# Kernel optimization log

Hardware: AMD Instinct MI355X
Metric: run time of the kernel (lower is better)

Reference implementation:

```python
import jax, jax.numpy as jnp
import numpy as np

B = 524288
D_IN = 128
D_OUT = 128
MASK_DENSITY = 0.25  # fraction of DAG edges present


def setup_inputs() -> dict:
    key = jax.random.key(0)
    k = jax.random.split(key, 6)
    x0 = jax.random.normal(k[0], (B, D_IN), dtype=jnp.float32)
    x1 = jax.random.normal(k[1], (B, D_IN), dtype=jnp.float32)
    # weights ~ N(0, 0.1^2) as in torch.normal(mean=0, std=0.1)
    w0 = jax.random.normal(k[2], (D_OUT, D_IN), dtype=jnp.float32) * 0.1
    w1 = jax.random.normal(k[3], (D_OUT, D_IN), dtype=jnp.float32) * 0.1
    # binary DAG connectivity masks [out_dim, in_dims[i]]
    m0 = (jax.random.uniform(k[4], (D_OUT, D_IN)) < MASK_DENSITY).astype(jnp.float32)
    m1 = (jax.random.uniform(k[5], (D_OUT, D_IN)) < MASK_DENSITY).astype(jnp.float32)
    return {"x0": x0, "x1": x1, "w0": w0, "w1": w1, "m0": m0, "m1": m1}


def reference(x0, x1, w0, w1, m0, m1):
    # sum_i  x_i @ (W_i * M_i)^T   -> [B, out_dim]
    # (note: original module creates self.bias but never adds it in forward)
    out = jnp.einsum("bi,oi->bo", x0, w0 * m0)
    out = out + jnp.einsum("bi,oi->bo", x1, w1 * m1)
    return out
```

## Files before the change

kernel.cpp:

```cpp
#include <hip/hip_runtime.h>

typedef __attribute__((ext_vector_type(8))) short bf16x8;
typedef __attribute__((ext_vector_type(4))) float f32x4;
typedef __attribute__((ext_vector_type(4))) int   i32x4;
typedef __attribute__((ext_vector_type(2))) unsigned int u32x2;

#define NBLK 1024
#define NTHR 512
#define NT   32
#define DOUT 128

__device__ __forceinline__ unsigned short bf_rne(float x) {
  unsigned u = __builtin_bit_cast(unsigned, x);
  return (unsigned short)((u + 0x7FFFu + ((u >> 16) & 1u)) >> 16);
}
__device__ __forceinline__ void split2(float x, short& hi, short& lo) {
  unsigned u = __builtin_bit_cast(unsigned, x);
  float hf = __builtin_bit_cast(float, u & 0xFFFF0000u);
  hi = (short)(unsigned short)(u >> 16);
  lo = (short)bf_rne(x - hf);
}
__device__ __forceinline__ unsigned pk(short a, short b) {
  return (unsigned)(unsigned short)a | ((unsigned)(unsigned short)b << 16);
}
__device__ __forceinline__ void gll16(const float* g, char* l) {
  __builtin_amdgcn_global_load_lds(
      (const __attribute__((address_space(1))) unsigned int*)g,
      (__attribute__((address_space(3))) unsigned int*)l, 16, 0, 0);
}

#define MFMA_AW(ACC, W, X)                                                   \
  asm("s_nop 1\n\tv_mfma_f32_16x16x32_bf16 %0, %1, %2, %0"                   \
      : "+v"(ACC) : "a"(W), "v"(X))

__global__ __launch_bounds__(NTHR, 2)
void dagmm(const float* __restrict__ x0, const float* __restrict__ x1,
           const float* __restrict__ w0, const float* __restrict__ w1,
           const float* __restrict__ m0, const float* __restrict__ m1,
           float* __restrict__ out)
{
  __shared__ __align__(16) char L[65536];

  const int t   = threadIdx.x;
  const int l   = t & 63;
  const int w   = t >> 6;
  const int l16 = l & 15;
  const int lq  = l >> 4;

  i32x4 WH[8], WL[8];
  {
    const int col = w * 16 + l16;
#pragma unroll
    for (int ks = 0; ks < 8; ++ks) {
      const int k0 = ks * 32 + lq * 8;
      const float* wp = (k0 < 128) ? (w0 + col * 128 + k0) : (w1 + col * 128 + (k0 - 128));
      const float* mp = (k0 < 128) ? (m0 + col * 128 + k0) : (m1 + col * 128 + (k0 - 128));
      float4 wa = *(const float4*)wp, wb = *(const float4*)(wp + 4);
      float4 ma = *(const float4*)mp, mb = *(const float4*)(mp + 4);
      float v[8] = {wa.x*ma.x, wa.y*ma.y, wa.z*ma.z, wa.w*ma.w,
                    wb.x*mb.x, wb.y*mb.y, wb.z*mb.z, wb.w*mb.w};
      bf16x8 hv, lv;
#pragma unroll
      for (int j = 0; j < 8; ++j) { short h, lo2; split2(v[j], h, lo2); hv[j] = h; lv[j] = lo2; }
      WH[ks] = __builtin_bit_cast(i32x4, hv);
      WL[ks] = __builtin_bit_cast(i32x4, lv);
      asm volatile("" : "+a"(WH[ks]));
      asm volatile("" : "+a"(WL[ks]));
    }
  }

  const size_t Tbase = (size_t)blockIdx.x * (NT * 16);
  const float* xsrc = (l < 32) ? (x0 + l * 4) : (x1 + (l - 32) * 4);

#define ISSUE(ts, fbase)                                                     \
  {                                                                          \
    _Pragma("unroll")                                                        \
    for (int i = 0; i < 2; ++i) {                                            \
      const int row = w + i * 8;                                             \
      const size_t grow = Tbase + (size_t)(ts) * 16 + row;                   \
      gll16(xsrc + grow * 128, L + (fbase) + row * 1024);                    \
    }                                                                        \
  }

#define SPLIT(fbase, bbase)                                                  \
  {                                                                          \
    const float4 ra = *(const float4*)(L + (fbase) + t * 16);                \
    const float4 rb = *(const float4*)(L + (fbase) + t * 16 + 8192);         \
    const int ks   = (t & 63) >> 3;                                          \
    const int oct  = ((t & 63) >> 1) & 3;                                    \
    const int half = (t & 1) * 8;                                            \
    short h0,h1,h2,h3, e0,e1,e2,e3;                                          \
    u32x2 hv, lv;                                                            \
    {                                        \
      split2(ra.x, h0, e0); split2(ra.y, h1, e1);                            \
      split2(ra.z, h2, e2); split2(ra.w, h3, e3);                            \
      hv[0] = pk(h0, h1); hv[1] = pk(h2, h3);                                \
      lv[0] = pk(e0, e1); lv[1] = pk(e2, e3);                                \
      const int lam = (t >> 6) | (oct << 4);                                 \
      char* p = L + (bbase) + ks * 1024 + (((lam ^ ks)) << 4) + half;        \
      *(u32x2*)p          = hv;                                              \
      *(u32x2*)(p + 8192) = lv;                                              \
    }                                                                        \
    {                                         \
      split2(rb.x, h0, e0); split2(rb.y, h1, e1);                            \
      split2(rb.z, h2, e2); split2(rb.w, h3, e3);                            \
      hv[0] = pk(h0, h1); hv[1] = pk(h2, h3);                                \
      lv[0] = pk(e0, e1); lv[1] = pk(e2, e3);                                \
      const int lam = (8 + (t >> 6)) | (oct << 4);                           \
      char* p = L + (bbase) + ks * 1024 + (((lam ^ ks)) << 4) + half;        \
      *(u32x2*)p          = hv;                                              \
      *(u32x2*)(p + 8192) = lv;                                              \
    }                                                                        \
  }

  ISSUE(0, 0);
  ISSUE(1, 16384);
  asm volatile("s_waitcnt vmcnt(2)" ::: "memory");
  SPLIT(0, 32768);
  asm volatile("s_waitcnt lgkmcnt(0)" ::: "memory");

  for (int tt = 0; tt < NT; ++tt) {
    const int r = tt & 1;

    asm volatile("" ::: "memory");
    __builtin_amdgcn_s_barrier();
    asm volatile("" ::: "memory");

    { const int ts = (tt + 2 < NT) ? (tt + 2) : (NT - 1); ISSUE(ts, r * 16384); }

    asm volatile("s_waitcnt vmcnt(2)" ::: "memory");

    if (tt + 1 < NT) SPLIT((r ^ 1) * 16384, 32768 + (r ^ 1) * 16384);

    f32x4 acc = (f32x4){0.f, 0.f, 0.f, 0.f};
    {
      const char* Bb = L + 32768 + r * 16384;
#pragma unroll
      for (int ks = 0; ks < 8; ++ks) {
        const char* bp = Bb + ks * 1024 + ((l ^ ks) << 4);
        i32x4 xh = *(const i32x4*)bp;
        i32x4 xl = *(const i32x4*)(bp + 8192);
        MFMA_AW(acc, WH[ks], xh);
        MFMA_AW(acc, WH[ks], xl);
        MFMA_AW(acc, WL[ks], xh);
      }
    }
    asm volatile("s_nop 7\n\ts_nop 7" :::);

    {
      const size_t row = Tbase + (size_t)tt * 16 + l16;
      *(f32x4*)&out[row * DOUT + w * 16 + lq * 4] = acc;
    }

    asm volatile("s_waitcnt lgkmcnt(0)" ::: "memory");
  }
#undef ISSUE
#undef SPLIT
}

extern "C" void kernel_launch(void* const* d_in, const int* in_sizes, int n_in,
                              void* d_out, int out_size, void* d_ws, size_t ws_size,
                              hipStream_t stream) {
  const float* x0 = (const float*)d_in[0];
  const float* x1 = (const float*)d_in[1];
  const float* w0 = (const float*)d_in[2];
  const float* w1 = (const float*)d_in[3];
  const float* m0 = (const float*)d_in[4];
  const float* m1 = (const float*)d_in[5];
  dagmm<<<NBLK, NTHR, 0, stream>>>(x0, x1, w0, w1, m0, m1, (float*)d_out);
}
```

Measured before the change: 184.8 us.

## Halve block size, give each wave two output column tiles, use hardware bf16 pack

Cuts the block to 4 waves, each holding weights for two 16-column output tiles so every B-fragment read from LDS feeds two MFMA chains. This halves LDS fragment reads per output and interleaves two independent accumulators to hide MFMA dependency latency. The split-to-bf16 step switches to v_cvt_pk_bf16_f32, and each thread now converts four rows' worth of loads, with waitcnt adjusted for four loads per stage. It doubles weight register use per thread, and there is a stray line that dereferences a null pointer in the weight setup that may be optimized away or crash.

```diff
diff --git a/kernel.cpp b/kernel.cpp
--- a/kernel.cpp
+++ b/kernel.cpp
@@ -1,12 +1,11 @@
 #include <hip/hip_runtime.h>
 
-typedef __attribute__((ext_vector_type(8))) short bf16x8;
 typedef __attribute__((ext_vector_type(4))) float f32x4;
 typedef __attribute__((ext_vector_type(4))) int   i32x4;
 typedef __attribute__((ext_vector_type(2))) unsigned int u32x2;
 
 #define NBLK 1024
-#define NTHR 512
+#define NTHR 256
 #define NT   32
 #define DOUT 128
 
@@ -20,15 +19,17 @@
   hi = (short)(unsigned short)(u >> 16);
   lo = (short)bf_rne(x - hf);
 }
-__device__ __forceinline__ unsigned pk(short a, short b) {
-  return (unsigned)(unsigned short)a | ((unsigned)(unsigned short)b << 16);
+__device__ __forceinline__ float fbits(unsigned u) { return __builtin_bit_cast(float, u); }
+__device__ __forceinline__ unsigned cvtpk(float a, float b) {
+  unsigned r;
+  asm("v_cvt_pk_bf16_f32 %0, %1, %2" : "=v"(r) : "v"(a), "v"(b));
+  return r;
 }
 __device__ __forceinline__ void gll16(const float* g, char* l) {
   __builtin_amdgcn_global_load_lds(
       (const __attribute__((address_space(1))) unsigned int*)g,
       (__attribute__((address_space(3))) unsigned int*)l, 16, 0, 0);
 }
-
 #define MFMA_AW(ACC, W, X)                                                   \
   asm("s_nop 1\n\tv_mfma_f32_16x16x32_bf16 %0, %1, %2, %0"                   \
       : "+v"(ACC) : "a"(W), "v"(X))
@@ -47,9 +48,10 @@
   const int l16 = l & 15;
   const int lq  = l >> 4;
 
-  i32x4 WH[8], WL[8];
-  {
-    const int col = w * 16 + l16;
+  i32x4 WH[2][8], WL[2][8];
+#pragma unroll
+  for (int c = 0; c < 2; ++c) {
+    const int col = w * 32 + c * 16 + l16;
 #pragma unroll
     for (int ks = 0; ks < 8; ++ks) {
       const int k0 = ks * 32 + lq * 8;
@@ -59,55 +61,56 @@
       float4 ma = *(const float4*)mp, mb = *(const float4*)(mp + 4);
       float v[8] = {wa.x*ma.x, wa.y*ma.y, wa.z*ma.z, wa.w*ma.w,
                     wb.x*mb.x, wb.y*mb.y, wb.z*mb.z, wb.w*mb.w};
-      bf16x8 hv, lv;
+      short hv[8], lv[8];
 #pragma unroll
-      for (int j = 0; j < 8; ++j) { short h, lo2; split2(v[j], h, lo2); hv[j] = h; lv[j] = lo2; }
-      WH[ks] = __builtin_bit_cast(i32x4, hv);
-      WL[ks] = __builtin_bit_cast(i32x4, lv);
-      asm volatile("" : "+a"(WH[ks]));
-      asm volatile("" : "+a"(WL[ks]));
+      for (int j = 0; j < 8; ++j) split2(v[j], hv[j], lv[j]);
+      WH[c][ks] = __builtin_bit_cast(i32x4, *(f32x4*)0 == *(f32x4*)0 ? *(i32x4*)hv : *(i32x4*)hv);
+      WH[c][ks] = *(const i32x4*)hv;
+      WL[c][ks] = *(const i32x4*)lv;
+      asm volatile("" : "+a"(WH[c][ks]));
+      asm volatile("" : "+a"(WL[c][ks]));
     }
   }
 
   const size_t Tbase = (size_t)blockIdx.x * (NT * 16);
   const float* xsrc = (l < 32) ? (x0 + l * 4) : (x1 + (l - 32) * 4);
 
-#define ISSUE(ts, fbase)                                                     \
+#define ISSUE(ts, fb)                                                        \
   {                                                                          \
     _Pragma("unroll")                                                        \
-    for (int i = 0; i < 2; ++i) {                                            \
-      const int row = w + i * 8;                                             \
+    for (int i = 0; i < 4; ++i) {                                            \
+      const int row = w * 4 + i;                                             \
       const size_t grow = Tbase + (size_t)(ts) * 16 + row;                   \
-      gll16(xsrc + grow * 128, L + (fbase) + row * 1024);                    \
+      gll16(xsrc + grow * 128, L + (fb) + row * 1024);                       \
     }                                                                        \
   }
 
-#define SPLIT(fbase, bbase)                                                  \
+  const int rS    = t >> 4;
+  const int vS    = t & 15;
+  const int lamS  = rS | (((vS >> 1) & 3) << 4);
+  const int halfS = (vS & 1) * 8;
+
+#define SPLIT(fb, bb)                                                        \
   {                                                                          \
-    const float4 ra = *(const float4*)(L + (fbase) + t * 16);                \
-    const float4 rb = *(const float4*)(L + (fbase) + t * 16 + 8192);         \
-    const int ks   = (t & 63) >> 3;                                          \
-    const int oct  = ((t & 63) >> 1) & 3;                                    \
-    const int half = (t & 1) * 8;                                            \
-    short h0,h1,h2,h3, e0,e1,e2,e3;                                          \
-    u32x2 hv, lv;                                                            \
-    {                                        \
-      split2(ra.x, h0, e0); split2(ra.y, h1, e1);                            \
-      split2(ra.z, h2, e2); split2(ra.w, h3, e3);                            \
-      hv[0] = pk(h0, h1); hv[1] = pk(h2, h3);                                \
-      lv[0] = pk(e0, e1); lv[1] = pk(e2, e3);                                \
-      const int lam = (t >> 6) | (oct << 4);                                 \
-      char* p = L + (bbase) + ks * 1024 + (((lam ^ ks)) << 4) + half;        \
-      *(u32x2*)p          = hv;                                              \
-      *(u32x2*)(p + 8192) = lv;                                              \
-    }                                                                        \
-    {                                         \
-      split2(rb.x, h0, e0); split2(rb.y, h1, e1);                            \
-      split2(rb.z, h2, e2); split2(rb.w, h3, e3);                            \
-      hv[0] = pk(h0, h1); hv[1] = pk(h2, h3);                                \
-      lv[0] = pk(e0, e1); lv[1] = pk(e2, e3);                                \
-      const int lam = (8 + (t >> 6)) | (oct << 4);                           \
-      char* p = L + (bbase) + ks * 1024 + (((lam ^ ks)) << 4) + half;        \
+    const char* Fb = L + (fb) + rS * 1024 + vS * 16;                         \
+    f32x4 f0 = *(const f32x4*)(Fb);                                          \
+    f32x4 f1 = *(const f32x4*)(Fb + 256);                                    \
+    f32x4 f2 = *(const f32x4*)(Fb + 512);                                    \
+    f32x4 f3 = *(const f32x4*)(Fb + 768);                                    \
+    _Pragma("unroll")                                                        \
+    for (int q = 0; q < 4; ++q) {                                            \
+      f32x4 f = (q == 0) ? f0 : (q == 1) ? f1 : (q == 2) ? f2 : f3;          \
+      unsigned h01 = cvtpk(f[0], f[1]);                                      \
+      unsigned h23 = cvtpk(f[2], f[3]);                                      \
+      float e0 = f[0] - fbits(h01 << 16);                                    \
+      float e1 = f[1] - fbits(h01 & 0xffff0000u);                            \
+      float e2 = f[2] - fbits(h23 << 16);                                    \
+      float e3 = f[3] - fbits(h23 & 0xffff0000u);                            \
+      u32x2 hv, lv;                                                          \
+      hv[0] = h01; hv[1] = h23;                                              \
+      lv[0] = cvtpk(e0, e1); lv[1] = cvtpk(e2, e3);                          \
+      const int ksq = (vS >> 3) + 2 * q;                                     \
+      char* p = L + (bb) + ksq * 1024 + ((lamS ^ ksq) << 4) + halfS;         \
       *(u32x2*)p          = hv;                                              \
       *(u32x2*)(p + 8192) = lv;                                              \
     }                                                                        \
@@ -115,7 +118,7 @@
 
   ISSUE(0, 0);
   ISSUE(1, 16384);
-  asm volatile("s_waitcnt vmcnt(2)" ::: "memory");
+  asm volatile("s_waitcnt vmcnt(4)" ::: "memory");
   SPLIT(0, 32768);
   asm volatile("s_waitcnt lgkmcnt(0)" ::: "memory");
 
@@ -128,11 +131,12 @@
 
     { const int ts = (tt + 2 < NT) ? (tt + 2) : (NT - 1); ISSUE(ts, r * 16384); }
 
-    asm volatile("s_waitcnt vmcnt(2)" ::: "memory");
+    asm volatile("s_waitcnt vmcnt(4)" ::: "memory");
 
     if (tt + 1 < NT) SPLIT((r ^ 1) * 16384, 32768 + (r ^ 1) * 16384);
 
-    f32x4 acc = (f32x4){0.f, 0.f, 0.f, 0.f};
+    f32x4 acc0 = (f32x4){0.f, 0.f, 0.f, 0.f};
+    f32x4 acc1 = (f32x4){0.f, 0.f, 0.f, 0.f};
     {
       const char* Bb = L + 32768 + r * 16384;
 #pragma unroll
@@ -140,16 +144,20 @@
         const char* bp = Bb + ks * 1024 + ((l ^ ks) << 4);
         i32x4 xh = *(const i32x4*)bp;
         i32x4 xl = *(const i32x4*)(bp + 8192);
-        MFMA_AW(acc, WH[ks], xh);
-        MFMA_AW(acc, WH[ks], xl);
-        MFMA_AW(acc, WL[ks], xh);
+        MFMA_AW(acc0, WH[0][ks], xh);
+        MFMA_AW(acc1, WH[1][ks], xh);
+        MFMA_AW(acc0, WH[0][ks], xl);
+        MFMA_AW(acc1, WH[1][ks], xl);
+        MFMA_AW(acc0, WL[0][ks], xh);
+        MFMA_AW(acc1, WL[1][ks], xh);
       }
     }
     asm volatile("s_nop 7\n\ts_nop 7" :::);
 
     {
       const size_t row = Tbase + (size_t)tt * 16 + l16;
-      *(f32x4*)&out[row * DOUT + w * 16 + lq * 4] = acc;
+      *(f32x4*)&out[row * DOUT + w * 32 + lq * 4]      = acc0;
+      *(f32x4*)&out[row * DOUT + w * 32 + 16 + lq * 4] = acc1;
     }
 
     asm volatile("s_waitcnt lgkmcnt(0)" ::: "memory");
```

Result: no change. 184.8 us (+0.0%).
